# Kernel optimization log

Measured on AMD Instinct MI355X. Metric: run time of the kernel, lower is better.

## Reference

```python
import jax, jax.numpy as jnp
import numpy as np

N_NODES, N_EDGES, N_ROOTS = 32768, 131072, 1024
VOCAB, EMB_D, FEAT = 50000, 256, 128
SEQ, HEADS, OUT_CH = 16, 16, 125
KERNELS = (5, 6, 7, 8)


def _add_self_loops(edge_index, n):
    loop = jnp.arange(n, dtype=edge_index.dtype)
    src = jnp.concatenate([edge_index[0], loop])
    dst = jnp.concatenate([edge_index[1], loop])
    return src, dst


def _gat_conv(x, W, a_src, a_dst, b, src, dst, n):
    # PyG GATConv (heads=1): h=xW, e_ij = LeakyReLU(a_s.h_j + a_d.h_i), softmax over incoming edges of i
    h = x @ W                                   # [N, F]
    al_s = h @ a_src                            # [N]
    al_d = h @ a_dst                            # [N]
    e = jax.nn.leaky_relu(al_s[src] + al_d[dst], 0.2)   # [E+N]
    m = jax.ops.segment_max(e, dst, num_segments=n)
    ex = jnp.exp(e - m[dst])
    den = jax.ops.segment_sum(ex, dst, num_segments=n)
    coef = ex / den[dst]
    out = jax.ops.segment_sum(coef[:, None] * h[src], dst, num_segments=n)
    return out + b


def _gcn_conv(x, W, b, src, dst, n):
    h = x @ W
    ones = jnp.ones_like(src, dtype=x.dtype)
    deg = jax.ops.segment_sum(ones, dst, num_segments=n)
    dinv = jax.lax.rsqrt(jnp.maximum(deg, 1.0))
    norm = dinv[src] * dinv[dst]                # [E+N]
    out = jax.ops.segment_sum(norm[:, None] * h[src], dst, num_segments=n)
    return out + b


def _transformer_block(x, Wq, bq, Wk, bk, Wv, bv, Wo, bo, g, be):
    # multi-head self-attention + output proj + residual + layernorm (attn_dropout=0)
    n, s, d = x.shape
    dh = d // HEADS
    q = (x @ Wq + bq).reshape(n, s, HEADS, dh)
    k = (x @ Wk + bk).reshape(n, s, HEADS, dh)
    v = (x @ Wv + bv).reshape(n, s, HEADS, dh)
    att = jnp.einsum('nqhd,nkhd->nhqk', q, k) / np.sqrt(dh).astype(np.float32)
    att = jax.nn.softmax(att, axis=-1)
    o = jnp.einsum('nhqk,nkhd->nqhd', att, v).reshape(n, s, d)
    o = o @ Wo + bo
    y = x + o
    mu = jnp.mean(y, axis=-1, keepdims=True)
    var = jnp.var(y, axis=-1, keepdims=True)
    return (y - mu) * jax.lax.rsqrt(var + 1e-5) * g + be


def _conv_branch(t, ws, bs):
    # t: [N, D, S]; Conv1d VALID + ReLU + max-pool over full output length
    feats = []
    for w, b in zip(ws, bs):
        a = jax.lax.conv_general_dilated(t, w, (1,), 'VALID',
                                         dimension_numbers=('NCH', 'OIH', 'NCH'))
        a = jax.nn.relu(a + b[:, None])
        feats.append(jnp.max(a, axis=-1))       # [N, OUT_CH]
    return jnp.concatenate(feats, axis=1)        # [N, 4*OUT_CH]


def _forward(x2, emb, Wq, bq, Wk, bk, Wv, bv, Wo, bo, ln_g, ln_b,
             gat1_W, gat1_as, gat1_ad, gat1_b, gcn1_W, gcn1_b,
             gat2_W, gat2_as, gat2_ad, gat2_b, gcn2_W, gcn2_b,
             conv_w0, conv_b0, conv_w1, conv_b1, conv_w2, conv_b2, conv_w3, conv_b3,
             fc1_W, fc1_b, fc2_W, fc2_b,
             text2, edge_index, root_index, rootpost_index):
    n = x2.shape[0]
    src, dst = _add_self_loops(edge_index, n)

    stance_graph = _gat_conv(x2, gat1_W, gat1_as, gat1_ad, gat1_b, src, dst, n)
    stance_shared = _gcn_conv(x2, gcn1_W, gcn1_b, src, dst, n)

    t = emb[text2]                                            # [N, S, D]
    t = _transformer_block(t, Wq, bq, Wk, bk, Wv, bv, Wo, bo, ln_g, ln_b)
    t_avg = jnp.mean(t, axis=1)                               # [N, D]

    cat = jnp.concatenate([stance_graph, stance_shared, t_avg], axis=1)  # [N, 2F+D]
    stance_graph2 = _gat_conv(cat, gat2_W, gat2_as, gat2_ad, gat2_b, src, dst, n)
    _ = _gcn_conv(stance_shared, gcn2_W, gcn2_b, src, dst, n)  # computed but unused in forward (faithful)

    tc = jnp.transpose(t, (0, 2, 1))                          # [N, D, S]
    text_feat = _conv_branch(tc, (conv_w0, conv_w1, conv_w2, conv_w3),
                             (conv_b0, conv_b1, conv_b2, conv_b3))  # [N, 500]

    final = jnp.concatenate([stance_graph2[root_index],
                             text_feat[root_index],
                             text_feat[rootpost_index]], axis=1)     # [B, F+1000]
    h = jax.nn.relu(final @ fc1_W + fc1_b)
    return h @ fc2_W + fc2_b                                  # [B, 3]


def setup_inputs() -> dict:
    key = jax.random.key(0)
    ks = iter(jax.random.split(key, 48))
    s = 0.05
    inp = {}
    inp['x2'] = jax.random.normal(next(ks), (N_NODES, FEAT), jnp.float32)
    inp['emb'] = jax.random.normal(next(ks), (VOCAB, EMB_D), jnp.float32) * s
    for nm in ['Wq', 'Wk', 'Wv', 'Wo']:
        inp[nm] = jax.random.normal(next(ks), (EMB_D, EMB_D), jnp.float32) * s
    for nm in ['bq', 'bk', 'bv', 'bo']:
        inp[nm] = jnp.zeros((EMB_D,), jnp.float32)
    inp['ln_g'] = jnp.ones((EMB_D,), jnp.float32)
    inp['ln_b'] = jnp.zeros((EMB_D,), jnp.float32)
    inp['gat1_W'] = jax.random.normal(next(ks), (FEAT, FEAT), jnp.float32) * s
    inp['gat1_as'] = jax.random.normal(next(ks), (FEAT,), jnp.float32) * s
    inp['gat1_ad'] = jax.random.normal(next(ks), (FEAT,), jnp.float32) * s
    inp['gat1_b'] = jnp.zeros((FEAT,), jnp.float32)
    inp['gcn1_W'] = jax.random.normal(next(ks), (FEAT, FEAT), jnp.float32) * s
    inp['gcn1_b'] = jnp.zeros((FEAT,), jnp.float32)
    inp['gat2_W'] = jax.random.normal(next(ks), (2 * FEAT + EMB_D, FEAT), jnp.float32) * s
    inp['gat2_as'] = jax.random.normal(next(ks), (FEAT,), jnp.float32) * s
    inp['gat2_ad'] = jax.random.normal(next(ks), (FEAT,), jnp.float32) * s
    inp['gat2_b'] = jnp.zeros((FEAT,), jnp.float32)
    inp['gcn2_W'] = jax.random.normal(next(ks), (FEAT, FEAT), jnp.float32) * s
    inp['gcn2_b'] = jnp.zeros((FEAT,), jnp.float32)
    for i, K in enumerate(KERNELS):
        inp[f'conv_w{i}'] = jax.random.normal(next(ks), (OUT_CH, EMB_D, K), jnp.float32) * s
        inp[f'conv_b{i}'] = jnp.zeros((OUT_CH,), jnp.float32)
    inp['fc1_W'] = jax.random.normal(next(ks), (FEAT + 8 * OUT_CH, 300), jnp.float32) * s
    inp['fc1_b'] = jnp.zeros((300,), jnp.float32)
    inp['fc2_W'] = jax.random.normal(next(ks), (300, 3), jnp.float32) * s
    inp['fc2_b'] = jnp.zeros((3,), jnp.float32)
    inp['text2'] = jax.random.randint(next(ks), (N_NODES, SEQ), 0, VOCAB, jnp.int32)
    inp['edge_index'] = jax.random.randint(next(ks), (2, N_EDGES), 0, N_NODES, jnp.int32)
    inp['root_index'] = jax.random.randint(next(ks), (N_ROOTS,), 0, N_NODES, jnp.int32)
    inp['rootpost_index'] = jax.random.randint(next(ks), (N_ROOTS,), 0, N_NODES, jnp.int32)
    return inp


def reference(x2, emb, Wq, bq, Wk, bk, Wv, bv, Wo, bo, ln_g, ln_b,
              gat1_W, gat1_as, gat1_ad, gat1_b, gcn1_W, gcn1_b,
              gat2_W, gat2_as, gat2_ad, gat2_b, gcn2_W, gcn2_b,
              conv_w0, conv_b0, conv_w1, conv_b1, conv_w2, conv_b2, conv_w3, conv_b3,
              fc1_W, fc1_b, fc2_W, fc2_b,
              text2, edge_index, root_index, rootpost_index):
    return _forward(x2, emb, Wq, bq, Wk, bk, Wv, bv, Wo, bo, ln_g, ln_b,
                    gat1_W, gat1_as, gat1_ad, gat1_b, gcn1_W, gcn1_b,
                    gat2_W, gat2_as, gat2_ad, gat2_b, gcn2_W, gcn2_b,
                    conv_w0, conv_b0, conv_w1, conv_b1, conv_w2, conv_b2, conv_w3, conv_b3,
                    fc1_W, fc1_b, fc2_W, fc2_b,
                    text2, edge_index, root_index, rootpost_index)
```

## Files before the change

### kernel.cpp

```cpp
#include <hip/hip_runtime.h>
#include <hip/hip_bf16.h>
#include <cstdint>
#include <cstddef>

#define N_NODES 32768
#define N_EDGES 131072
#define ET_EDGES (N_EDGES + N_NODES)
#define N_ROOTS 1024
#define EMB_D 256
#define FEAT 128
#define SEQ 16
#define OUT_CH 125

static inline int cdiv(long long a, long long b) { return (int)((a + b - 1) / b); }

typedef short short8 __attribute__((ext_vector_type(8)));
typedef short short4v __attribute__((ext_vector_type(4)));
typedef float f32x4 __attribute__((ext_vector_type(4)));

__device__ __forceinline__ float warpReduceSum(float v) {
#pragma unroll
    for (int m = 32; m; m >>= 1) v += __shfl_xor(v, m, 64);
    return v;
}
__device__ __forceinline__ int encf(float f) {
    int i = __float_as_int(f);
    return i >= 0 ? i : (i ^ 0x7fffffff);
}
__device__ __forceinline__ float decf(int i) {
    return __int_as_float(i >= 0 ? i : (i ^ 0x7fffffff));
}
__device__ __forceinline__ short f2bs(float x) {
    unsigned u = __float_as_uint(x);
    u += 0x7fffu + ((u >> 16) & 1u);
    return (short)(u >> 16);
}
__device__ __forceinline__ short2 f2bs2(float a, float b) {
    union {
        __hip_bfloat162 h;
        short2 s;
    } u;
    u.h = __float22bfloat162_rn(make_float2(a, b));
    return u.s;
}
__device__ __forceinline__ float bs2f(short s) {
    return __uint_as_float(((unsigned)(unsigned short)s) << 16);
}

__global__ void fill_i32(int* p, int v, int n) {
    int i = blockIdx.x * 256 + threadIdx.x;
    if (i < n) p[i] = v;
}

__global__ void init_cat(float* __restrict__ cat, const float* __restrict__ b1, const float* __restrict__ b2) {
    int i = blockIdx.x * 256 + threadIdx.x;
    int n = i >> 8, c = i & 255;
    float b = (c < 128) ? b1[c] : b2[c - 128];
    cat[(size_t)n * 512 + c] = b;
}

__global__ void repack_wall(const float* __restrict__ cw0, const float* __restrict__ cw1,
                            const float* __restrict__ cw2, const float* __restrict__ cw3,
                            __hip_bfloat16* __restrict__ wall) {
    int i = blockIdx.x * 256 + threadIdx.x;
    if (i >= 512 * 2048) return;
    int r = i >> 11, c = i & 2047;
    int k = c >> 8, ic = c & 255;
    float v = 0.f;
    if (r < 500) {
        int Kidx = r / 125, oc = r - Kidx * 125;
        int K = 5 + Kidx;
        if (k < K) {
            const float* cw = Kidx == 0 ? cw0 : Kidx == 1 ? cw1 : Kidx == 2 ? cw2 : cw3;
            v = cw[((size_t)oc * 256 + ic) * K + k];
        }
    }
    wall[i] = __float2bfloat16(v);
}

__global__ void repack_xf(const float* __restrict__ Wq, const float* __restrict__ Wk, const float* __restrict__ Wv,
                          const float* __restrict__ Wo, const float* __restrict__ bq, const float* __restrict__ bk,
                          const float* __restrict__ bv, short* __restrict__ wqkvT, short* __restrict__ woT,
                          float* __restrict__ bqkv) {
    int i = blockIdx.x * 256 + threadIdx.x;
    if (i < 768 * 256) {
        int n = i >> 8, k = i & 255;
        const float* W = n < 256 ? Wq : n < 512 ? Wk : Wv;
        wqkvT[i] = f2bs(W[k * 256 + (n & 255)]);
    }
    if (i < 256 * 256) {
        int n = i >> 8, k = i & 255;
        woT[i] = f2bs(Wo[k * 256 + n]);
    }
    if (i < 768) bqkv[i] = i < 256 ? bq[i] : i < 512 ? bk[i - 256] : bv[i - 512];
}

__global__ void repack_wT(const float* __restrict__ W, short* __restrict__ out, int K, int N) {
    int i = blockIdx.x * 256 + threadIdx.x;
    if (i >= K * N) return;
    int n = i / K, k = i - n * K;
    out[i] = f2bs(W[(size_t)k * N + n]);
}

__global__ __launch_bounds__(256) void mfma_gemm_n128(const float* __restrict__ A, const short* __restrict__ Wt,
                                                      float* __restrict__ C, int K) {
    __shared__ short As[128 * 40];
    __shared__ short Bs[128 * 40];
    const int m0 = blockIdx.x * 128;
    const int tid = threadIdx.x;
    const int lane = tid & 63;
    const int wave = tid >> 6;
    const int wm = (wave >> 1) * 64, wn = (wave & 1) * 64;
    const int quad = lane >> 4, l16 = lane & 15;

    const int r0 = tid >> 2, kc = (tid & 3) * 8;
    const int r1 = r0 + 64;

    f32x4 acc[4][4];
#pragma unroll
    for (int i = 0; i < 4; i++)
#pragma unroll
        for (int j = 0; j < 4; j++) acc[i][j] = (f32x4){0.f, 0.f, 0.f, 0.f};

    for (int k0 = 0; k0 < K; k0 += 32) {
#pragma unroll
        for (int rr = 0; rr < 2; rr++) {
            const int r = rr ? r1 : r0;
            const float* pa = A + (size_t)(m0 + r) * K + k0 + kc;
            float4 a0 = ((const float4*)pa)[0], a1 = ((const float4*)pa)[1];
            short2 c0 = f2bs2(a0.x, a0.y), c1 = f2bs2(a0.z, a0.w), c2 = f2bs2(a1.x, a1.y), c3 = f2bs2(a1.z, a1.w);
            *(short8*)(As + r * 40 + kc) = (short8){c0.x, c0.y, c1.x, c1.y, c2.x, c2.y, c3.x, c3.y};
        }
        *(short8*)(Bs + r0 * 40 + kc) = *(const short8*)(Wt + (size_t)r0 * K + k0 + kc);
        *(short8*)(Bs + r1 * 40 + kc) = *(const short8*)(Wt + (size_t)r1 * K + k0 + kc);
        __syncthreads();
        short8 af[4], bfr[4];
#pragma unroll
        for (int i = 0; i < 4; i++) af[i] = *(const short8*)(As + (wm + i * 16 + l16) * 40 + quad * 8);
#pragma unroll
        for (int j = 0; j < 4; j++) bfr[j] = *(const short8*)(Bs + (wn + j * 16 + l16) * 40 + quad * 8);
#pragma unroll
        for (int i = 0; i < 4; i++)
#pragma unroll
            for (int j = 0; j < 4; j++)
                acc[i][j] = __builtin_amdgcn_mfma_f32_16x16x32_bf16(af[i], bfr[j], acc[i][j], 0, 0, 0);
        __syncthreads();
    }
#pragma unroll
    for (int i = 0; i < 4; i++) {
#pragma unroll
        for (int j = 0; j < 4; j++) {
            const int col = wn + j * 16 + l16;
            const size_t base = (size_t)(m0 + wm + i * 16 + quad * 4) * 128 + col;
#pragma unroll
            for (int r = 0; r < 4; r++) C[base + (size_t)r * 128] = acc[i][j][r];
        }
    }
}

__global__ __launch_bounds__(256) void gemm64(const float* __restrict__ A, const float* __restrict__ B,
                                              const float* __restrict__ bias, float* __restrict__ C,
                                              int M, int N, int K, int lda, int ldc, int doRelu) {
    __shared__ float As[16][65];
    __shared__ float Bs[16][65];
    const int bm = blockIdx.y * 64, bn = blockIdx.x * 64;
    const int tid = threadIdx.x;
    const int tx = tid & 15, ty = tid >> 4;
    float acc[4][4] = {};
    for (int k0 = 0; k0 < K; k0 += 16) {
#pragma unroll
        for (int j = 0; j < 4; j++) {
            int i = tid + j * 256;
            int kk = i & 15, m = i >> 4;
            int gr = bm + m, gc = k0 + kk;
            As[kk][m] = (gr < M && gc < K) ? A[(size_t)gr * lda + gc] : 0.f;
        }
#pragma unroll
        for (int j = 0; j < 4; j++) {
            int i = tid + j * 256;
            int n = i & 63, kk = i >> 6;
            int gr = k0 + kk, gc = bn + n;
            Bs[kk][n] = (gr < K && gc < N) ? B[(size_t)gr * N + gc] : 0.f;
        }
        __syncthreads();
#pragma unroll
        for (int kk = 0; kk < 16; kk++) {
            float a[4], b[4];
#pragma unroll
            for (int i2 = 0; i2 < 4; i2++) a[i2] = As[kk][ty * 4 + i2];
#pragma unroll
            for (int j2 = 0; j2 < 4; j2++) b[j2] = Bs[kk][tx * 4 + j2];
#pragma unroll
            for (int i2 = 0; i2 < 4; i2++)
#pragma unroll
                for (int j2 = 0; j2 < 4; j2++) acc[i2][j2] = fmaf(a[i2], b[j2], acc[i2][j2]);
        }
        __syncthreads();
    }
#pragma unroll
    for (int i2 = 0; i2 < 4; i2++) {
        int r = bm + ty * 4 + i2;
        if (r >= M) continue;
#pragma unroll
        for (int j2 = 0; j2 < 4; j2++) {
            int c = bn + tx * 4 + j2;
            if (c >= N) continue;
            float v = acc[i2][j2];
            if (bias) v += bias[c];
            if (doRelu) v = fmaxf(v, 0.f);
            C[(size_t)r * ldc + c] = v;
        }
    }
}

__global__ __launch_bounds__(256) void alpha_kernel(const float* __restrict__ h, const float* __restrict__ asrc,
                                                    const float* __restrict__ adst, float* __restrict__ als,
                                                    float* __restrict__ ald) {
    int gw = (blockIdx.x * 256 + threadIdx.x) >> 6;
    int lane = threadIdx.x & 63;
    if (gw >= N_NODES) return;
    const float* row = h + (size_t)gw * FEAT;
    float v0 = row[lane], v1 = row[lane + 64];
    float ps = v0 * asrc[lane] + v1 * asrc[lane + 64];
    float pd = v0 * adst[lane] + v1 * adst[lane + 64];
    ps = warpReduceSum(ps);
    pd = warpReduceSum(pd);
    if (lane == 0) {
        als[gw] = ps;
        ald[gw] = pd;
    }
}

__device__ __forceinline__ void edge_decode(int i, const int* __restrict__ ei, int& s, int& d) {
    if (i < N_EDGES) {
        s = ei[i];
        d = ei[N_EDGES + i];
    } else {
        s = d = i - N_EDGES;
    }
}

__global__ void edge_p1(const int* __restrict__ ei, const float* __restrict__ als, const float* __restrict__ ald,
                        float* __restrict__ elog, int* __restrict__ menc, float* dega) {
    int i = blockIdx.x * 256 + threadIdx.x;
    if (i >= ET_EDGES) return;
    int s, d;
    edge_decode(i, ei, s, d);
    float e = als[s] + ald[d];
    e = (e >= 0.f) ? e : 0.2f * e;
    elog[i] = e;
    atomicMax(&menc[d], encf(e));
    if (dega) unsafeAtomicAdd(&dega[d], 1.f);
}

__global__ void edge_p2(const int* __restrict__ ei, float* __restrict__ elog, const int* __restrict__ menc,
                        float* __restrict__ den) {
    int i = blockIdx.x * 256 + threadIdx.x;
    if (i >= ET_EDGES) return;
    int s, d;
    edge_decode(i, ei, s, d);
    float ex = __expf(elog[i] - decf(menc[d]));
    elog[i] = ex;
    unsafeAtomicAdd(&den[d], ex);
}

__global__ void edge_p2b(const int* __restrict__ ei, float* __restrict__ elog, const float* __restrict__ den) {
    int i = blockIdx.x * 256 + threadIdx.x;
    if (i >= ET_EDGES) return;
    int s, d;
    edge_decode(i, ei, s, d);
    elog[i] = elog[i] / den[d];
}

__global__ void dinv_kernel(float* deg) {
    int i = blockIdx.x * 256 + threadIdx.x;
    if (i < N_NODES) deg[i] = rsqrtf(fmaxf(deg[i], 1.f));
}

__global__ void edge_scatter(const int* __restrict__ ei, const float* __restrict__ coef, const float* __restrict__ h,
                             float* __restrict__ out, int ldo) {
    int i = blockIdx.x * 256 + threadIdx.x;
    if (i >= ET_EDGES * FEAT) return;
    int e = i >> 7, f = i & 127;
    int s, d;
    edge_decode(e, ei, s, d);
    unsafeAtomicAdd(&out[(size_t)d * ldo + f], coef[e] * h[(size_t)s * FEAT + f]);
}

__global__ void gcn_scatter(const int* __restrict__ ei, const float* __restrict__ dinv, const float* __restrict__ h,
                            float* __restrict__ out, int ldo) {
    int i = blockIdx.x * 256 + threadIdx.x;
    if (i >= ET_EDGES * FEAT) return;
    int e = i >> 7, f = i & 127;
    int s, d;
    edge_decode(e, ei, s, d);
    float coef = dinv[s] * dinv[d];
    unsafeAtomicAdd(&out[(size_t)d * ldo + f], coef * h[(size_t)s * FEAT + f]);
}

__global__ void root_gather(const float* __restrict__ g2, const int* __restrict__ rooti, const float* __restrict__ gb,
                            float* __restrict__ fin) {
    int i = blockIdx.x * 256 + threadIdx.x;
    if (i >= N_ROOTS * FEAT) return;
    int r = i >> 7, c = i & 127;
    fin[(size_t)r * 1128 + c] = g2[(size_t)rooti[r] * FEAT + c] + gb[c];
}

__global__ void fc2_kernel(const float* __restrict__ fch, const float* __restrict__ W, const float* __restrict__ b,
                           float* __restrict__ out) {
    int i = blockIdx.x * 256 + threadIdx.x;
    if (i >= N_ROOTS * 3) return;
    int r = i / 3, c = i - r * 3;
    float acc = b[c];
    for (int k = 0; k < 300; k++) acc = fmaf(fch[(size_t)r * 300 + k], W[k * 3 + c], acc);
    out[i] = acc;
}

__device__ __forceinline__ int lsw(int row, int col) {
    return row * 256 + (col ^ ((row & 7) << 3));
}

__device__ __forceinline__ int vt_addr(int d, int key) {
    return d * 32 + (((key & 24) ^ (((d ^ (d >> 2)) & 3) << 3)) | (key & 7));
}

template <int MODE>
__global__ __launch_bounds__(256) void xformer_kernel(
    const float* __restrict__ emb, const int* __restrict__ text2, const short* __restrict__ wqkvT,
    const float* __restrict__ bqkv, const short* __restrict__ woT, const float* __restrict__ bo,
    const float* __restrict__ lng, const float* __restrict__ lnb, const int* __restrict__ rooti,
    const int* __restrict__ rpi, float* __restrict__ cat, unsigned short* __restrict__ tbuf) {
    __shared__ short qa[32 * 256];
    __shared__ short kreg[32 * 256];

    const int tid = threadIdx.x;
    const int wave = tid >> 6, lane = tid & 63;
    const int quad = lane >> 4, l16 = lane & 15;

    int gnode[2];
#pragma unroll
    for (int m = 0; m < 2; m++) {
        int slot = blockIdx.x * 2 + m;
        gnode[m] = (MODE == 0) ? slot : ((slot < N_ROOTS) ? rooti[slot] : rpi[slot - N_ROOTS]);
    }

    float4 ev[8];

    {
        const int row = tid >> 3, seg = tid & 7;
        const int m = row >> 4, r = row & 15;
        const int tok = text2[gnode[m] * SEQ + r];
        const float* ep = emb + (size_t)tok * 256 + seg * 32;
#pragma unroll
        for (int j = 0; j < 4; j++) {
            float4 ea = ((const float4*)(ep + j * 8))[0];
            float4 eb = ((const float4*)(ep + j * 8))[1];
            ev[j * 2] = ea;
            ev[j * 2 + 1] = eb;
            short2 w0 = f2bs2(ea.x, ea.y), w1 = f2bs2(ea.z, ea.w);
            short2 w2 = f2bs2(eb.x, eb.y), w3 = f2bs2(eb.z, eb.w);
            *(short8*)(kreg + lsw(row, seg * 32 + j * 8)) =
                (short8){w0.x, w0.y, w1.x, w1.y, w2.x, w2.y, w3.x, w3.y};
        }
    }
    __syncthreads();

    auto run_gemm = [&](const short* __restrict__ W, int wrow0, const short* __restrict__ Albase,
                        f32x4(&acc)[4][2]) {
#pragma unroll
        for (int i = 0; i < 4; i++) {
            acc[i][0] = (f32x4){0.f, 0.f, 0.f, 0.f};
            acc[i][1] = (f32x4){0.f, 0.f, 0.f, 0.f};
        }
        const short* wb = W + (size_t)(wrow0 + l16) * 256 + quad * 8;
        short8 Bcur[4], Bnxt[4];
#pragma unroll
        for (int i = 0; i < 4; i++) Bcur[i] = *(const short8*)(wb + (size_t)i * 16 * 256);
#pragma unroll
        for (int k0 = 0; k0 < 8; k0++) {
            if (k0 < 7) {
#pragma unroll
                for (int i = 0; i < 4; i++)
                    Bnxt[i] = *(const short8*)(wb + (size_t)i * 16 * 256 + (k0 + 1) * 32);
            }
            short8 A0 = *(const short8*)(Albase + lsw(l16, k0 * 32 + quad * 8));
            short8 A1 = *(const short8*)(Albase + lsw(16 + l16, k0 * 32 + quad * 8));
#pragma unroll
            for (int i = 0; i < 4; i++) {
                acc[i][0] = __builtin_amdgcn_mfma_f32_16x16x32_bf16(A0, Bcur[i], acc[i][0], 0, 0, 0);
                acc[i][1] = __builtin_amdgcn_mfma_f32_16x16x32_bf16(A1, Bcur[i], acc[i][1], 0, 0, 0);
            }
#pragma unroll
            for (int i = 0; i < 4; i++) Bcur[i] = Bnxt[i];
        }
    };

    f32x4 vacc[4][2];
    {
        f32x4 acc[4][2];
        run_gemm(wqkvT, (0 * 16 + wave * 4) * 16, kreg, acc);
#pragma unroll
        for (int i = 0; i < 4; i++) {
            const int col = (wave * 4 + i) * 16 + l16;
            const float b = bqkv[col];
#pragma unroll
            for (int m = 0; m < 2; m++) {
                const int rbase = m * 16 + quad * 4;
                short2 p01 = f2bs2((acc[i][m][0] + b) * 0.25f, (acc[i][m][1] + b) * 0.25f);
                short2 p23 = f2bs2((acc[i][m][2] + b) * 0.25f, (acc[i][m][3] + b) * 0.25f);
                qa[lsw(rbase + 0, col)] = p01.x;
                qa[lsw(rbase + 1, col)] = p01.y;
                qa[lsw(rbase + 2, col)] = p23.x;
                qa[lsw(rbase + 3, col)] = p23.y;
            }
        }
        run_gemm(wqkvT, (2 * 16 + wave * 4) * 16, kreg, vacc);
#pragma unroll
        for (int i = 0; i < 4; i++) {
            const float b = bqkv[(2 * 16 + wave * 4 + i) * 16 + l16];
#pragma unroll
            for (int m = 0; m < 2; m++)
#pragma unroll
                for (int r = 0; r < 4; r++) vacc[i][m][r] += b;
        }
        f32x4 kacc[4][2];
        run_gemm(wqkvT, (1 * 16 + wave * 4) * 16, kreg, kacc);
        __syncthreads();
#pragma unroll
        for (int i = 0; i < 4; i++) {
            const int colg = (1 * 16 + wave * 4 + i) * 16 + l16;
            const float b = bqkv[colg];
            const int cl = colg - 256;
#pragma unroll
            for (int m = 0; m < 2; m++) {
                const int rbase = m * 16 + quad * 4;
                short2 p01 = f2bs2(kacc[i][m][0] + b, kacc[i][m][1] + b);
                short2 p23 = f2bs2(kacc[i][m][2] + b, kacc[i][m][3] + b);
                kreg[lsw(rbase + 0, cl)] = p01.x;
                kreg[lsw(rbase + 1, cl)] = p01.y;
                kreg[lsw(rbase + 2, cl)] = p23.x;
                kreg[lsw(rbase + 3, cl)] = p23.y;
            }
        }
    }

#pragma unroll
    for (int p = 0; p < 2; p++) {
#pragma unroll
        for (int i = 0; i < 4; i++) {
            const int h = wave * 4 + i;
            const int arow = p * 16 + l16;
            const int q8 = (quad & 1) * 8;
            short8 Af = *(const short8*)(kreg + lsw(arow, h * 16 + q8));
            short8 Bf = *(const short8*)(qa + lsw(arow, h * 16 + q8));
            if (quad >= 2) {
                Af = (short8){0, 0, 0, 0, 0, 0, 0, 0};
                Bf = (short8){0, 0, 0, 0, 0, 0, 0, 0};
            }
            f32x4 S = __builtin_amdgcn_mfma_f32_16x16x32_bf16(Af, Bf, (f32x4){0.f, 0.f, 0.f, 0.f}, 0, 0, 0);
            float mx = fmaxf(fmaxf(S[0], S[1]), fmaxf(S[2], S[3]));
            mx = fmaxf(mx, __shfl_xor(mx, 16));
            mx = fmaxf(mx, __shfl_xor(mx, 32));
            float e0 = __expf(S[0] - mx), e1 = __expf(S[1] - mx);
            float e2 = __expf(S[2] - mx), e3 = __expf(S[3] - mx);
            float sm = (e0 + e1) + (e2 + e3);
            sm += __shfl_xor(sm, 16);
            sm += __shfl_xor(sm, 32);
            const float inv = 1.f / sm;
            short2 p01 = f2bs2(e0 * inv, e1 * inv), p23 = f2bs2(e2 * inv, e3 * inv);
            *(short4v*)(qa + lsw(arow, h * 16 + quad * 4)) = (short4v){p01.x, p01.y, p23.x, p23.y};
        }
    }
    __syncthreads();

#pragma unroll
    for (int i = 0; i < 4; i++) {
        const int d = (wave * 4 + i) * 16 + l16;
#pragma unroll
        for (int m = 0; m < 2; m++) {
            const int rbase = m * 16 + quad * 4;
            short2 p01 = f2bs2(vacc[i][m][0], vacc[i][m][1]), p23 = f2bs2(vacc[i][m][2], vacc[i][m][3]);
            *(short4v*)(kreg + vt_addr(d, rbase)) = (short4v){p01.x, p01.y, p23.x, p23.y};
        }
    }

#pragma unroll
    for (int p = 0; p < 2; p++) {
#pragma unroll
        for (int i = 0; i < 4; i++) {
            const int h = wave * 4 + i;
            const int arow = p * 16 + l16;
            const int q8 = (quad & 1) * 8;
            short8 BP = *(const short8*)(qa + lsw(arow, h * 16 + q8));
            short8 Av = *(const short8*)(kreg + vt_addr(h * 16 + l16, p * 16 + q8));
            if (quad >= 2) {
                BP = (short8){0, 0, 0, 0, 0, 0, 0, 0};
                Av = (short8){0, 0, 0, 0, 0, 0, 0, 0};
            }
            f32x4 O = __builtin_amdgcn_mfma_f32_16x16x32_bf16(Av, BP, (f32x4){0.f, 0.f, 0.f, 0.f}, 0, 0, 0);
            short2 o01 = f2bs2(O[0], O[1]), o23 = f2bs2(O[2], O[3]);
            *(short4v*)(qa + lsw(arow, h * 16 + quad * 4)) = (short4v){o01.x, o01.y, o23.x, o23.y};
        }
    }
    __syncthreads();

    {
        f32x4 oacc[4][2];
        run_gemm(woT, (wave * 4) * 16, qa, oacc);
#pragma unroll
        for (int i = 0; i < 4; i++) {
            const int col = (wave * 4 + i) * 16 + l16;
            const float bocol = bo[col];
#pragma unroll
            for (int m = 0; m < 2; m++) {
                const int rbase = m * 16 + quad * 4;
                short2 a01 = f2bs2(oacc[i][m][0] + bocol, oacc[i][m][1] + bocol);
                short2 a23 = f2bs2(oacc[i][m][2] + bocol, oacc[i][m][3] + bocol);
                kreg[lsw(rbase + 0, col)] = a01.x;
                kreg[lsw(rbase + 1, col)] = a01.y;
                kreg[lsw(rbase + 2, col)] = a23.x;
                kreg[lsw(rbase + 3, col)] = a23.y;
            }
        }
    }
    __syncthreads();

    float* qs = (float*)qa;
    {
        const int row = tid >> 3, seg = tid & 7;
        float sum = 0.f, sq = 0.f;
#pragma unroll
        for (int j = 0; j < 4; j++) {
            const int base = lsw(row, seg * 32 + j * 8);
            short8 y8 = *(const short8*)(kreg + base);
            float4 ea = ev[j * 2];
            float4 eb = ev[j * 2 + 1];
            float evv[8] = {ea.x, ea.y, ea.z, ea.w, eb.x, eb.y, eb.z, eb.w};
            float yv[8];
#pragma unroll
            for (int e = 0; e < 8; e++) {
                yv[e] = bs2f(y8[e]) + evv[e];
                sum += yv[e];
                sq = fmaf(yv[e], yv[e], sq);
            }
            short2 w0 = f2bs2(yv[0], yv[1]), w1 = f2bs2(yv[2], yv[3]);
            short2 w2 = f2bs2(yv[4], yv[5]), w3 = f2bs2(yv[6], yv[7]);
            *(short4v*)(kreg + base) = (short4v){w0.x, w0.y, w1.x, w1.y};
            *(short4v*)(kreg + base + 4) = (short4v){w2.x, w2.y, w3.x, w3.y};
        }
        qs[tid] = sum;
        qs[256 + tid] = sq;
    }
    __syncthreads();
    if (tid < 32) {
        float s = 0.f, q2 = 0.f;
#pragma unroll
        for (int j = 0; j < 8; j++) {
            s += qs[tid * 8 + j];
            q2 += qs[256 + tid * 8 + j];
        }
        float mu = s * (1.f / 256.f);
        float var = q2 * (1.f / 256.f) - mu * mu;
        qs[512 + tid * 2] = mu;
        qs[512 + tid * 2 + 1] = rsqrtf(var + 1e-5f);
    }
    __syncthreads();
    {
        const int c = tid;
        const float g = lng[c], bb = lnb[c];
        float csum[2] = {0.f, 0.f};
#pragma unroll
        for (int m = 0; m < 2; m++) {
#pragma unroll
            for (int r = 0; r < 16; r++) {
                const int row = m * 16 + r;
                const float yv = bs2f(kreg[lsw(row, c)]);
                const float mu = qs[512 + row * 2], rstd = qs[512 + row * 2 + 1];
                const float o = (yv - mu) * rstd * g + bb;
                if (MODE == 0) {
                    csum[m] += o;
                } else {
                    tbuf[((size_t)(blockIdx.x * 2 + m) * 24 + r) * 256 + c] = (unsigned short)f2bs(o);
                }
            }
        }
        if (MODE == 0) {
            cat[(size_t)gnode[0] * 512 + 256 + c] = csum[0] * (1.f / 16.f);
            cat[(size_t)gnode[1] * 512 + 256 + c] = csum[1] * (1.f / 16.f);
        } else {
            for (int z = tid; z < 2 * 8 * 256; z += 256) {
                const int m = z >> 11, rem = z & 2047;
                tbuf[((size_t)(blockIdx.x * 2 + m) * 24 + 16 + (rem >> 8)) * 256 + (rem & 255)] = 0;
            }
        }
    }
}

__global__ __launch_bounds__(256) void conv_gemm(const short* __restrict__ tb, const short* __restrict__ wall,
                                                 float* __restrict__ C) {
    __shared__ short As[128 * 40];
    __shared__ short Bs[128 * 40];
    const int bid = blockIdx.x;
    const int m0 = (bid >> 2) * 128;
    const int n0 = (bid & 3) * 128;
    const int tid = threadIdx.x;
    const int lane = tid & 63;
    const int wave = tid >> 6;
    const int wm = (wave >> 1) * 64, wn = (wave & 1) * 64;
    const int quad = lane >> 4, l16 = lane & 15;

    const int r0 = tid >> 2, kc = (tid & 3) * 8;
    const int r1 = r0 + 64;
    const int am0 = m0 + r0, am1 = m0 + r1;
    const int s0 = am0 / 12, p0_ = am0 - s0 * 12;
    const int s1 = am1 / 12, p1_ = am1 - s1 * 12;
    const size_t ga0 = (size_t)(s0 * 24 + p0_) * 256 + kc;
    const size_t ga1 = (size_t)(s1 * 24 + p1_) * 256 + kc;
    const size_t gb0 = (size_t)(n0 + r0) * 2048 + kc;
    const size_t gb1 = (size_t)(n0 + r1) * 2048 + kc;
    short* sa0 = As + r0 * 40 + kc;
    short* sa1 = As + r1 * 40 + kc;
    short* sb0 = Bs + r0 * 40 + kc;
    short* sb1 = Bs + r1 * 40 + kc;

    f32x4 acc[4][4];
#pragma unroll
    for (int i = 0; i < 4; i++)
#pragma unroll
        for (int j = 0; j < 4; j++) acc[i][j] = (f32x4){0.f, 0.f, 0.f, 0.f};

    for (int k0 = 0; k0 < 2048; k0 += 32) {
        short8 a0 = *(const short8*)(tb + ga0 + k0);
        short8 a1 = *(const short8*)(tb + ga1 + k0);
        short8 b0 = *(const short8*)(wall + gb0 + k0);
        short8 b1 = *(const short8*)(wall + gb1 + k0);
        *(short8*)sa0 = a0;
        *(short8*)sa1 = a1;
        *(short8*)sb0 = b0;
        *(short8*)sb1 = b1;
        __syncthreads();
        short8 af[4], bfr[4];
#pragma unroll
        for (int i = 0; i < 4; i++) af[i] = *(const short8*)(As + (wm + i * 16 + l16) * 40 + quad * 8);
#pragma unroll
        for (int j = 0; j < 4; j++) bfr[j] = *(const short8*)(Bs + (wn + j * 16 + l16) * 40 + quad * 8);
#pragma unroll
        for (int i = 0; i < 4; i++)
#pragma unroll
            for (int j = 0; j < 4; j++)
                acc[i][j] = __builtin_amdgcn_mfma_f32_16x16x32_bf16(af[i], bfr[j], acc[i][j], 0, 0, 0);
        __syncthreads();
    }
#pragma unroll
    for (int i = 0; i < 4; i++) {
#pragma unroll
        for (int j = 0; j < 4; j++) {
            const int col = n0 + wn + j * 16 + l16;
            const size_t base = (size_t)(m0 + wm + i * 16 + quad * 4) * 512 + col;
#pragma unroll
            for (int r = 0; r < 4; r++) C[base + (size_t)r * 512] = acc[i][j][r];
        }
    }
}

__global__ void conv_maxpool(const float* __restrict__ C, const float* __restrict__ cb0, const float* __restrict__ cb1,
                             const float* __restrict__ cb2, const float* __restrict__ cb3, float* __restrict__ fin) {
    int i = blockIdx.x * 256 + threadIdx.x;
    if (i >= 2048 * 500) return;
    int slot = i / 500, q = i - slot * 500;
    int Kidx = q / 125, oc = q - Kidx * 125;
    int L = 12 - Kidx;
    const float* base = C + (size_t)(slot * 12) * 512 + q;
    float m = base[0];
    for (int p = 1; p < L; p++) m = fmaxf(m, base[(size_t)p * 512]);
    float b = (Kidx == 0 ? cb0 : Kidx == 1 ? cb1 : Kidx == 2 ? cb2 : cb3)[oc];
    float v = fmaxf(m + b, 0.f);
    int idx = slot < N_ROOTS ? slot : slot - N_ROOTS;
    int colbase = slot < N_ROOTS ? 128 : 628;
    fin[(size_t)idx * 1128 + colbase + q] = v;
}

extern "C" void kernel_launch(void* const* d_in, const int* in_sizes, int n_in, void* d_out, int out_size, void* d_ws,
                              size_t ws_size, hipStream_t stream) {
    const float* x2 = (const float*)d_in[0];
    const float* emb = (const float*)d_in[1];
    const float* Wq = (const float*)d_in[2];
    const float* Wk = (const float*)d_in[3];
    const float* Wv = (const float*)d_in[4];
    const float* Wo = (const float*)d_in[5];
    const float* bq = (const float*)d_in[6];
    const float* bk = (const float*)d_in[7];
    const float* bv = (const float*)d_in[8];
    const float* bo = (const float*)d_in[9];
    const float* lng = (const float*)d_in[10];
    const float* lnb = (const float*)d_in[11];
    const float* gat1_W = (const float*)d_in[12];
    const float* gat1_as = (const float*)d_in[13];
    const float* gat1_ad = (const float*)d_in[14];
    const float* gat1_b = (const float*)d_in[15];
    const float* gcn1_W = (const float*)d_in[16];
    const float* gcn1_b = (const float*)d_in[17];
    const float* gat2_W = (const float*)d_in[18];
    const float* gat2_as = (const float*)d_in[19];
    const float* gat2_ad = (const float*)d_in[20];
    const float* gat2_b = (const float*)d_in[21];
    const float* cw0 = (const float*)d_in[24];
    const float* cb0 = (const float*)d_in[25];
    const float* cw1 = (const float*)d_in[26];
    const float* cb1 = (const float*)d_in[27];
    const float* cw2 = (const float*)d_in[28];
    const float* cb2 = (const float*)d_in[29];
    const float* cw3 = (const float*)d_in[30];
    const float* cb3 = (const float*)d_in[31];
    const float* fc1_W = (const float*)d_in[32];
    const float* fc1_b = (const float*)d_in[33];
    const float* fc2_W = (const float*)d_in[34];
    const float* fc2_b = (const float*)d_in[35];
    const int* text2 = (const int*)d_in[36];
    const int* ei = (const int*)d_in[37];
    const int* rooti = (const int*)d_in[38];
    const int* rpi = (const int*)d_in[39];

    float* ws = (float*)d_ws;
    size_t off = 0;
    auto alloc = [&](size_t n) {
        float* p = ws + off;
        off += n;
        return p;
    };
    float* g2o = alloc((size_t)N_NODES * FEAT);
    float* den1 = alloc(N_NODES);
    float* den2 = alloc(N_NODES);
    float* deg = alloc(N_NODES);
    size_t zero_floats = off;
    float* cat = alloc((size_t)N_NODES * 512);
    float* h1 = alloc((size_t)N_NODES * FEAT);
    float* h2 = alloc((size_t)N_NODES * FEAT);
    float* hg2 = alloc((size_t)N_NODES * FEAT);
    float* als1 = alloc(N_NODES);
    float* ald1 = alloc(N_NODES);
    float* als2 = alloc(N_NODES);
    float* ald2 = alloc(N_NODES);
    int* m1 = (int*)alloc(N_NODES);
    int* m2 = (int*)alloc(N_NODES);
    float* el1 = alloc(ET_EDGES);
    float* el2 = alloc(ET_EDGES);
    float* fin = alloc((size_t)N_ROOTS * 1128);
    float* fch = alloc((size_t)N_ROOTS * 300);
    float* wallf = alloc(512 * 2048 / 2);
    float* wqkvTf = alloc(768 * 256 / 2);
    float* woTf = alloc(256 * 256 / 2);
    float* bqkv = alloc(768);
    float* wg1Tf = alloc(128 * 128 / 2);
    float* wc1Tf = alloc(128 * 128 / 2);
    float* wg2Tf = alloc(128 * 512 / 2);
    (void)ws_size;
    (void)in_sizes;
    (void)n_in;
    (void)out_size;

    unsigned short* tbuf = (unsigned short*)h1;
    __hip_bfloat16* wall = (__hip_bfloat16*)wallf;
    short* wqkvT = (short*)wqkvTf;
    short* woT = (short*)woTf;
    short* wg1T = (short*)wg1Tf;
    short* wc1T = (short*)wc1Tf;
    short* wg2T = (short*)wg2Tf;
    float* Cbuf = cat;

    hipMemsetAsync(g2o, 0, zero_floats * sizeof(float), stream);
    init_cat<<<cdiv((long long)N_NODES * 256, 256), 256, 0, stream>>>(cat, gat1_b, gcn1_b);
    fill_i32<<<cdiv(2 * N_NODES, 256), 256, 0, stream>>>(m1, (int)0x80000000, 2 * N_NODES);
    repack_wall<<<cdiv(512 * 2048, 256), 256, 0, stream>>>(cw0, cw1, cw2, cw3, wall);
    repack_xf<<<cdiv(768 * 256, 256), 256, 0, stream>>>(Wq, Wk, Wv, Wo, bq, bk, bv, wqkvT, woT, bqkv);
    repack_wT<<<cdiv(128 * 128, 256), 256, 0, stream>>>(gat1_W, wg1T, 128, 128);
    repack_wT<<<cdiv(128 * 128, 256), 256, 0, stream>>>(gcn1_W, wc1T, 128, 128);
    repack_wT<<<cdiv(512 * 128, 256), 256, 0, stream>>>(gat2_W, wg2T, 512, 128);

    mfma_gemm_n128<<<N_NODES / 128, 256, 0, stream>>>(x2, wg1T, h1, 128);
    mfma_gemm_n128<<<N_NODES / 128, 256, 0, stream>>>(x2, wc1T, h2, 128);
    alpha_kernel<<<cdiv((long long)N_NODES * 64, 256), 256, 0, stream>>>(h1, gat1_as, gat1_ad, als1, ald1);
    edge_p1<<<cdiv(ET_EDGES, 256), 256, 0, stream>>>(ei, als1, ald1, el1, m1, deg);
    edge_p2<<<cdiv(ET_EDGES, 256), 256, 0, stream>>>(ei, el1, m1, den1);
    edge_p2b<<<cdiv(ET_EDGES, 256), 256, 0, stream>>>(ei, el1, den1);
    dinv_kernel<<<cdiv(N_NODES, 256), 256, 0, stream>>>(deg);
    const int sc_blocks = cdiv((long long)ET_EDGES * FEAT, 256);
    edge_scatter<<<sc_blocks, 256, 0, stream>>>(ei, el1, h1, cat + 0, 512);
    gcn_scatter<<<sc_blocks, 256, 0, stream>>>(ei, deg, h2, cat + 128, 512);
    xformer_kernel<0><<<N_NODES / 2, 256, 0, stream>>>(emb, text2, wqkvT, bqkv, woT, bo, lng, lnb, rooti, rpi, cat,
                                                       nullptr);
    xformer_kernel<1><<<2 * N_ROOTS / 2, 256, 0, stream>>>(emb, text2, wqkvT, bqkv, woT, bo, lng, lnb, rooti, rpi,
                                                           nullptr, tbuf);
    mfma_gemm_n128<<<N_NODES / 128, 256, 0, stream>>>(cat, wg2T, hg2, 512);
    alpha_kernel<<<cdiv((long long)N_NODES * 64, 256), 256, 0, stream>>>(hg2, gat2_as, gat2_ad, als2, ald2);
    edge_p1<<<cdiv(ET_EDGES, 256), 256, 0, stream>>>(ei, als2, ald2, el2, m2, nullptr);
    edge_p2<<<cdiv(ET_EDGES, 256), 256, 0, stream>>>(ei, el2, m2, den2);
    edge_p2b<<<cdiv(ET_EDGES, 256), 256, 0, stream>>>(ei, el2, den2);
    edge_scatter<<<sc_blocks, 256, 0, stream>>>(ei, el2, hg2, g2o, FEAT);
    conv_gemm<<<192 * 4, 256, 0, stream>>>((const short*)tbuf, (const short*)wall, Cbuf);
    root_gather<<<cdiv(N_ROOTS * FEAT, 256), 256, 0, stream>>>(g2o, rooti, gat2_b, fin);
    conv_maxpool<<<cdiv(2048 * 500, 256), 256, 0, stream>>>(Cbuf, cb0, cb1, cb2, cb3, fin);
    gemm64<<<dim3(cdiv(300, 64), cdiv(N_ROOTS, 64)), 256, 0, stream>>>(fin, fc1_W, fc1_b, fch, N_ROOTS, 300, 1128,
                                                                       1128, 300, 1);
    fc2_kernel<<<cdiv(N_ROOTS * 3, 256), 256, 0, stream>>>(fch, fc2_W, fc2_b, (float*)d_out);
}
```

Baseline: 2.322 ms.

## Cut transformer kernel register pressure with a separate K buffer and embedding reload

Adds a third shared-memory buffer that holds K, so V can be computed after K and written transposed right away instead of staying live in registers through the score/softmax phase. The embedding residual is re-read from global memory at layernorm time rather than kept in 32 registers. The launch bounds now request 4 blocks per CU. The goal is fewer live VGPRs and higher occupancy, paid for with 16KB more LDS per block and a second embedding gather. The extra LDS may itself cap occupancy.

Result: slower. 2.375 ms (+2.3%).

```diff
diff --git a/kernel.cpp b/kernel.cpp
--- a/kernel.cpp
+++ b/kernel.cpp
@@ -325,13 +325,14 @@
 }
 
 template <int MODE>
-__global__ __launch_bounds__(256) void xformer_kernel(
+__global__ __launch_bounds__(256, 4) void xformer_kernel(
     const float* __restrict__ emb, const int* __restrict__ text2, const short* __restrict__ wqkvT,
     const float* __restrict__ bqkv, const short* __restrict__ woT, const float* __restrict__ bo,
     const float* __restrict__ lng, const float* __restrict__ lnb, const int* __restrict__ rooti,
     const int* __restrict__ rpi, float* __restrict__ cat, unsigned short* __restrict__ tbuf) {
     __shared__ short qa[32 * 256];
     __shared__ short kreg[32 * 256];
+    __shared__ short vbuf[32 * 256];
 
     const int tid = threadIdx.x;
     const int wave = tid >> 6, lane = tid & 63;
@@ -343,8 +344,6 @@
         int slot = blockIdx.x * 2 + m;
         gnode[m] = (MODE == 0) ? slot : ((slot < N_ROOTS) ? rooti[slot] : rpi[slot - N_ROOTS]);
     }
-
-    float4 ev[8];
 
     {
         const int row = tid >> 3, seg = tid & 7;
@@ -355,8 +354,6 @@
         for (int j = 0; j < 4; j++) {
             float4 ea = ((const float4*)(ep + j * 8))[0];
             float4 eb = ((const float4*)(ep + j * 8))[1];
-            ev[j * 2] = ea;
-            ev[j * 2 + 1] = eb;
             short2 w0 = f2bs2(ea.x, ea.y), w1 = f2bs2(ea.z, ea.w);
             short2 w2 = f2bs2(eb.x, eb.y), w3 = f2bs2(eb.z, eb.w);
             *(short8*)(kreg + lsw(row, seg * 32 + j * 8)) =
@@ -395,7 +392,6 @@
         }
     };
 
-    f32x4 vacc[4][2];
     {
         f32x4 acc[4][2];
         run_gemm(wqkvT, (0 * 16 + wave * 4) * 16, kreg, acc);
@@ -414,18 +410,8 @@
                 qa[lsw(rbase + 3, col)] = p23.y;
             }
         }
-        run_gemm(wqkvT, (2 * 16 + wave * 4) * 16, kreg, vacc);
-#pragma unroll
-        for (int i = 0; i < 4; i++) {
-            const float b = bqkv[(2 * 16 + wave * 4 + i) * 16 + l16];
-#pragma unroll
-            for (int m = 0; m < 2; m++)
-#pragma unroll
-                for (int r = 0; r < 4; r++) vacc[i][m][r] += b;
-        }
         f32x4 kacc[4][2];
         run_gemm(wqkvT, (1 * 16 + wave * 4) * 16, kreg, kacc);
-        __syncthreads();
 #pragma unroll
         for (int i = 0; i < 4; i++) {
             const int colg = (1 * 16 + wave * 4 + i) * 16 + l16;
@@ -436,10 +422,25 @@
                 const int rbase = m * 16 + quad * 4;
                 short2 p01 = f2bs2(kacc[i][m][0] + b, kacc[i][m][1] + b);
                 short2 p23 = f2bs2(kacc[i][m][2] + b, kacc[i][m][3] + b);
-                kreg[lsw(rbase + 0, cl)] = p01.x;
-                kreg[lsw(rbase + 1, cl)] = p01.y;
-                kreg[lsw(rbase + 2, cl)] = p23.x;
-                kreg[lsw(rbase + 3, cl)] = p23.y;
+                vbuf[lsw(rbase + 0, cl)] = p01.x;
+                vbuf[lsw(rbase + 1, cl)] = p01.y;
+                vbuf[lsw(rbase + 2, cl)] = p23.x;
+                vbuf[lsw(rbase + 3, cl)] = p23.y;
+            }
+        }
+        f32x4 vacc[4][2];
+        run_gemm(wqkvT, (2 * 16 + wave * 4) * 16, kreg, vacc);
+        __syncthreads();
+#pragma unroll
+        for (int i = 0; i < 4; i++) {
+            const int d = (wave * 4 + i) * 16 + l16;
+            const float b = bqkv[(2 * 16 + wave * 4 + i) * 16 + l16];
+#pragma unroll
+            for (int m = 0; m < 2; m++) {
+                const int rbase = m * 16 + quad * 4;
+                short2 p01 = f2bs2(vacc[i][m][0] + b, vacc[i][m][1] + b);
+                short2 p23 = f2bs2(vacc[i][m][2] + b, vacc[i][m][3] + b);
+                *(short4v*)(kreg + vt_addr(d, rbase)) = (short4v){p01.x, p01.y, p23.x, p23.y};
             }
         }
     }
@@ -451,7 +452,7 @@
             const int h = wave * 4 + i;
             const int arow = p * 16 + l16;
             const int q8 = (quad & 1) * 8;
-            short8 Af = *(const short8*)(kreg + lsw(arow, h * 16 + q8));
+            short8 Af = *(const short8*)(vbuf + lsw(arow, h * 16 + q8));
             short8 Bf = *(const short8*)(qa + lsw(arow, h * 16 + q8));
             if (quad >= 2) {
                 Af = (short8){0, 0, 0, 0, 0, 0, 0, 0};
@@ -471,18 +472,6 @@
             *(short4v*)(qa + lsw(arow, h * 16 + quad * 4)) = (short4v){p01.x, p01.y, p23.x, p23.y};
         }
     }
-    __syncthreads();
-
-#pragma unroll
-    for (int i = 0; i < 4; i++) {
-        const int d = (wave * 4 + i) * 16 + l16;
-#pragma unroll
-        for (int m = 0; m < 2; m++) {
-            const int rbase = m * 16 + quad * 4;
-            short2 p01 = f2bs2(vacc[i][m][0], vacc[i][m][1]), p23 = f2bs2(vacc[i][m][2], vacc[i][m][3]);
-            *(short4v*)(kreg + vt_addr(d, rbase)) = (short4v){p01.x, p01.y, p23.x, p23.y};
-        }
-    }
 
 #pragma unroll
     for (int p = 0; p < 2; p++) {
@@ -528,13 +517,16 @@
     float* qs = (float*)qa;
     {
         const int row = tid >> 3, seg = tid & 7;
+        const int m = row >> 4, r = row & 15;
+        const int tokr = text2[gnode[m] * SEQ + r];
+        const float* ep = emb + (size_t)tokr * 256 + seg * 32;
         float sum = 0.f, sq = 0.f;
 #pragma unroll
         for (int j = 0; j < 4; j++) {
             const int base = lsw(row, seg * 32 + j * 8);
             short8 y8 = *(const short8*)(kreg + base);
-            float4 ea = ev[j * 2];
-            float4 eb = ev[j * 2 + 1];
+            float4 ea = ((const float4*)(ep + j * 8))[0];
+            float4 eb = ((const float4*)(ep + j * 8))[1];
             float evv[8] = {ea.x, ea.y, ea.z, ea.w, eb.x, eb.y, eb.z, eb.w};
             float yv[8];
 #pragma unroll
```
